# Kernel tuning notes

Hardware: AMD Instinct MI355X
Metric: run time of the kernel (lower is better)

## Reference

```python
import jax, jax.numpy as jnp
import numpy as np

N = 16384      # nodes
E = 524288     # edges (avg degree 32)
F_IN, H1, H2 = 256, 64, 32


def _spmm(edge_src, edge_dst, edge_weight, h):
    """Sparse A @ h with A given as COO edge list: out[i] = sum_{e: src==i} w_e * h[dst_e]."""
    msg = h[edge_dst] * edge_weight[:, None]          # [E, d] gather + scale
    return jax.ops.segment_sum(msg, edge_src, num_segments=N)


def setup_inputs() -> dict:
    key = jax.random.key(0)
    ks = jax.random.split(key, 9)
    x = jax.random.normal(ks[0], (N, F_IN), dtype=jnp.float32)
    edge_src = jax.random.randint(ks[1], (E,), 0, N, dtype=jnp.int32)
    edge_dst = jax.random.randint(ks[2], (E,), 0, N, dtype=jnp.int32)
    edge_weight = jax.random.uniform(ks[3], (E,), dtype=jnp.float32)
    # Xavier-uniform GCN weights
    def xavier(k, shape):
        lim = np.sqrt(6.0 / (shape[0] + shape[1])).astype(np.float32)
        return jax.random.uniform(k, shape, jnp.float32, -lim, lim)
    W1 = xavier(ks[4], (F_IN, H1))
    W2 = xavier(ks[5], (H1, H2))
    W3 = xavier(ks[6], (H1, H2))
    R = jax.random.normal(ks[7], (H2,), dtype=jnp.float32)           # DEDICOM diagonal
    M = jnp.diag(jax.random.normal(ks[8], (H2,), dtype=jnp.float32))  # initialized as diag(randn)
    return dict(x=x, edge_weight=edge_weight, W1=W1, W2=W2, W3=W3, R=R, M=M,
                edge_src=edge_src, edge_dst=edge_dst)


def reference(x, edge_weight, W1, W2, W3, R, M, edge_src, edge_dst):
    # GCN propagation A @ (X @ W); stored activations are never applied in the
    # original ConvGraph.forward, so none are applied here. Eval mode: no
    # dropout, reparameterize returns z_mean.
    h = _spmm(edge_src, edge_dst, edge_weight, x @ W1)        # [N, H1]
    z_mean = _spmm(edge_src, edge_dst, edge_weight, h @ W2)   # [N, H2]
    z_log_std = _spmm(edge_src, edge_dst, edge_weight, h @ W3)
    z = z_mean
    # DEDICOM decoder (act = identity): zt = z @ diag(R) @ M @ diag(R); out = zt @ zt.T
    zt = ((z * R[None, :]) @ M) * R[None, :]                  # diag matmuls -> elementwise scales
    adj_pred = zt @ zt.T                                      # [N, N]
    return adj_pred, z_mean, z_log_std
```

## Files before the change

kernel.cpp:

```cpp
#include <hip/hip_runtime.h>
#include <hip/hip_bf16.h>

#define NN 16384
#define NE 524288
#define FIN 256
#define HH1 64
#define HH2 32

typedef __attribute__((ext_vector_type(8))) short bf16x8;
typedef __attribute__((ext_vector_type(4))) float f32x4;

__global__ __launch_bounds__(256) void zero_ints(int* __restrict__ p, int n) {
  int i = blockIdx.x * 256 + threadIdx.x;
  if (i < n) p[i] = 0;
}

__global__ __launch_bounds__(256) void gemm_xw1(const float* __restrict__ x,
                                                const float* __restrict__ W1,
                                                float* __restrict__ H0) {
  __shared__ float xs[64][65];
  __shared__ float ws[64][65];
  const int t = threadIdx.x;
  const int row0 = blockIdx.x * 64;
  const int tr = t >> 4, tc = t & 15;
  float acc[4][4] = {};
  for (int kc = 0; kc < FIN; kc += 64) {
#pragma unroll
    for (int i = 0; i < 4; ++i) {
      int slot = t + i * 256;
      int r = slot >> 4, c4 = (slot & 15) * 4;
      float4 v = *reinterpret_cast<const float4*>(&x[(size_t)(row0 + r) * FIN + kc + c4]);
      xs[r][c4 + 0] = v.x; xs[r][c4 + 1] = v.y; xs[r][c4 + 2] = v.z; xs[r][c4 + 3] = v.w;
      float4 wv = *reinterpret_cast<const float4*>(&W1[(size_t)(kc + r) * HH1 + c4]);
      ws[r][c4 + 0] = wv.x; ws[r][c4 + 1] = wv.y; ws[r][c4 + 2] = wv.z; ws[r][c4 + 3] = wv.w;
    }
    __syncthreads();
#pragma unroll
    for (int k = 0; k < 64; ++k) {
      float a[4], b[4];
#pragma unroll
      for (int i = 0; i < 4; ++i) a[i] = xs[tr * 4 + i][k];
#pragma unroll
      for (int j = 0; j < 4; ++j) b[j] = ws[k][tc * 4 + j];
#pragma unroll
      for (int i = 0; i < 4; ++i)
#pragma unroll
        for (int j = 0; j < 4; ++j) acc[i][j] += a[i] * b[j];
    }
    __syncthreads();
  }
#pragma unroll
  for (int i = 0; i < 4; ++i) {
    float4 o; o.x = acc[i][0]; o.y = acc[i][1]; o.z = acc[i][2]; o.w = acc[i][3];
    *reinterpret_cast<float4*>(&H0[(size_t)(row0 + tr * 4 + i) * HH1 + tc * 4]) = o;
  }
}

__global__ __launch_bounds__(256) void hist_src(const int* __restrict__ src,
                                                int* __restrict__ cnt) {
  int e = blockIdx.x * 256 + threadIdx.x;
  if (e < NE) atomicAdd(&cnt[src[e]], 1);
}

__global__ __launch_bounds__(256) void scan_offsets(const int* __restrict__ cnt,
                                                    int* __restrict__ off,
                                                    int* __restrict__ cur) {
  __shared__ int wsum[4];
  __shared__ int wpre[4];
  const int t = threadIdx.x;
  const int lane = t & 63, w = t >> 6;
  int v[64];
#pragma unroll
  for (int i = 0; i < 16; ++i) {
    int4 q = reinterpret_cast<const int4*>(cnt)[t * 16 + i];
    v[i * 4 + 0] = q.x; v[i * 4 + 1] = q.y; v[i * 4 + 2] = q.z; v[i * 4 + 3] = q.w;
  }
  int s = 0;
#pragma unroll
  for (int i = 0; i < 64; ++i) s += v[i];
  int incl = s;
#pragma unroll
  for (int d = 1; d < 64; d <<= 1) {
    int n = __shfl_up(incl, d, 64);
    if (lane >= d) incl += n;
  }
  if (lane == 63) wsum[w] = incl;
  __syncthreads();
  if (t == 0) {
    int run = 0;
    for (int i = 0; i < 4; ++i) { int x = wsum[i]; wpre[i] = run; run += x; }
  }
  __syncthreads();
  int run = incl - s + wpre[w];
#pragma unroll
  for (int i = 0; i < 16; ++i) {
    int4 o;
    o.x = run; run += v[i * 4 + 0];
    o.y = run; run += v[i * 4 + 1];
    o.z = run; run += v[i * 4 + 2];
    o.w = run; run += v[i * 4 + 3];
    reinterpret_cast<int4*>(off)[t * 16 + i] = o;
    reinterpret_cast<int4*>(cur)[t * 16 + i] = o;
  }
  if (t == 255) off[NN] = run;
}

__global__ __launch_bounds__(256) void scatter_edges(const int* __restrict__ src,
                                                     const int* __restrict__ dst,
                                                     const float* __restrict__ w,
                                                     int* __restrict__ cur,
                                                     int* __restrict__ sdst,
                                                     float* __restrict__ sw) {
  int e = blockIdx.x * 256 + threadIdx.x;
  if (e < NE) {
    int s = src[e];
    int p = atomicAdd(&cur[s], 1);
    sdst[p] = dst[e];
    sw[p] = w[e];
  }
}

__global__ __launch_bounds__(256) void spmm_g(const int* __restrict__ off,
                                              const int* __restrict__ sdst,
                                              const float* __restrict__ sw,
                                              const float* __restrict__ Hin,
                                              const float* __restrict__ W2,
                                              const float* __restrict__ W3,
                                              float* __restrict__ G) {
  __shared__ float wsh[64][64];
  __shared__ float hsh[4][64];
  const int t = threadIdx.x;
  for (int i = t; i < 64 * 32; i += 256) {
    int k = i >> 5, c = i & 31;
    wsh[k][c]      = W2[i];
    wsh[k][c + 32] = W3[i];
  }
  const int node = blockIdx.x * 4 + (t >> 6);
  const int lane = t & 63;
  const int beg = off[node], end = off[node + 1];
  float acc = 0.f;
  int e = beg;
  for (; e + 4 <= end; e += 4) {
    int d0 = sdst[e], d1 = sdst[e + 1], d2 = sdst[e + 2], d3 = sdst[e + 3];
    float w0 = sw[e], w1 = sw[e + 1], w2 = sw[e + 2], w3 = sw[e + 3];
    acc += w0 * Hin[(size_t)d0 * 64 + lane];
    acc += w1 * Hin[(size_t)d1 * 64 + lane];
    acc += w2 * Hin[(size_t)d2 * 64 + lane];
    acc += w3 * Hin[(size_t)d3 * 64 + lane];
  }
  for (; e < end; ++e) acc += sw[e] * Hin[(size_t)sdst[e] * 64 + lane];
  hsh[t >> 6][lane] = acc;
  __syncthreads();
  float g = 0.f;
#pragma unroll
  for (int k = 0; k < 64; ++k) g += hsh[t >> 6][k] * wsh[k][lane];
  G[(size_t)node * 64 + lane] = g;
}

__global__ __launch_bounds__(256) void spmm_zt(const int* __restrict__ off,
                                               const int* __restrict__ sdst,
                                               const float* __restrict__ sw,
                                               const float* __restrict__ G,
                                               const float* __restrict__ R,
                                               const float* __restrict__ M,
                                               float* __restrict__ zmean,
                                               float* __restrict__ zlog,
                                               __hip_bfloat16* __restrict__ ztb) {
  __shared__ float Ms[32][33];
  __shared__ float zr[4][32];
  const int t = threadIdx.x;
  for (int i = t; i < 1024; i += 256) Ms[i >> 5][i & 31] = M[i];
  const int wv = t >> 6, lane = t & 63;
  const int node = blockIdx.x * 4 + wv;
  const int beg = off[node], end = off[node + 1];
  float acc = 0.f;
  int e = beg;
  for (; e + 4 <= end; e += 4) {
    int d0 = sdst[e], d1 = sdst[e + 1], d2 = sdst[e + 2], d3 = sdst[e + 3];
    float w0 = sw[e], w1 = sw[e + 1], w2 = sw[e + 2], w3 = sw[e + 3];
    acc += w0 * G[(size_t)d0 * 64 + lane];
    acc += w1 * G[(size_t)d1 * 64 + lane];
    acc += w2 * G[(size_t)d2 * 64 + lane];
    acc += w3 * G[(size_t)d3 * 64 + lane];
  }
  for (; e < end; ++e) acc += sw[e] * G[(size_t)sdst[e] * 64 + lane];
  if (lane < 32) {
    zmean[(size_t)node * 32 + lane] = acc;
    zr[wv][lane] = acc * R[lane];
  } else {
    zlog[(size_t)node * 32 + (lane - 32)] = acc;
  }
  __syncthreads();
  if (lane < 32) {
    float zt = 0.f;
#pragma unroll
    for (int k = 0; k < 32; ++k) zt += zr[wv][k] * Ms[k][lane];
    ztb[(size_t)node * 32 + lane] = __float2bfloat16(zt * R[lane]);
  }
}

__global__ __launch_bounds__(256) void adj_mfma(const __hip_bfloat16* __restrict__ ztb,
                                                float* __restrict__ adj) {
  __shared__ float lds[4][16][128];
  const int wave = threadIdx.x >> 6;
  const int lane = threadIdx.x & 63;
  const int l15 = lane & 15;
  const int kblk = lane >> 4;
  const int rbase = blockIdx.y * 64 + wave * 16;
  const int cbase = blockIdx.x * 128;
  const short* zs = reinterpret_cast<const short*>(ztb);

  bf16x8 b0 = *reinterpret_cast<const bf16x8*>(&zs[(size_t)(rbase + l15) * 32 + kblk * 8]);

#pragma unroll
  for (int tc = 0; tc < 8; ++tc) {
    bf16x8 a = *reinterpret_cast<const bf16x8*>(
        &zs[(size_t)(cbase + tc * 16 + l15) * 32 + kblk * 8]);
    f32x4 z4 = {0.f, 0.f, 0.f, 0.f};
    f32x4 d = __builtin_amdgcn_mfma_f32_16x16x32_bf16(a, b0, z4, 0, 0, 0);
    int unit = (tc * 4 + kblk) ^ (l15 & 7);
    *reinterpret_cast<f32x4*>(&lds[wave][l15][unit * 4]) = d;
  }

  const int j = lane & 7;
#pragma unroll
  for (int rg = 0; rg < 2; ++rg) {
    const int rl = rg * 8 + (lane >> 3);
    float* dst = &adj[(size_t)(rbase + rl) * NN + cbase];
#pragma unroll
    for (int it = 0; it < 4; ++it) {
      int unit = (it * 8 + j) ^ (rl & 7);
      f32x4 v = *reinterpret_cast<const f32x4*>(&lds[wave][rl][unit * 4]);
      *reinterpret_cast<f32x4*>(dst + it * 32 + j * 4) = v;
    }
  }
}

extern "C" void kernel_launch(void* const* d_in, const int* in_sizes, int n_in,
                              void* d_out, int out_size, void* d_ws, size_t ws_size,
                              hipStream_t stream) {
  (void)in_sizes; (void)n_in; (void)out_size; (void)ws_size;

  const float* x   = (const float*)d_in[0];
  const float* ew  = (const float*)d_in[1];
  const float* W1  = (const float*)d_in[2];
  const float* W2  = (const float*)d_in[3];
  const float* W3  = (const float*)d_in[4];
  const float* R   = (const float*)d_in[5];
  const float* M   = (const float*)d_in[6];
  const int* esrc  = (const int*)d_in[7];
  const int* edst  = (const int*)d_in[8];

  float* adj_out   = (float*)d_out;
  float* zmean_out = adj_out + (size_t)NN * NN;
  float* zlog_out  = zmean_out + (size_t)NN * HH2;

  char* p = (char*)d_ws;
  float* H0 = (float*)p;                 p += (size_t)NN * HH1 * 4;
  float* G  = (float*)p;                 p += (size_t)NN * HH1 * 4;
  __hip_bfloat16* ztb = (__hip_bfloat16*)p; p += (size_t)NN * HH2 * 2;
  int* cnt  = (int*)p;                   p += (size_t)NN * 4;
  int* off  = (int*)p;                   p += (size_t)(NN + 4) * 4;
  int* cur  = (int*)p;                   p += (size_t)NN * 4;
  int* sdst = (int*)p;                   p += (size_t)NE * 4;
  float* sw = (float*)p;                 p += (size_t)NE * 4;

  zero_ints<<<NN / 256, 256, 0, stream>>>(cnt, NN);
  gemm_xw1<<<NN / 64, 256, 0, stream>>>(x, W1, H0);
  hist_src<<<NE / 256, 256, 0, stream>>>(esrc, cnt);
  scan_offsets<<<1, 256, 0, stream>>>(cnt, off, cur);
  scatter_edges<<<NE / 256, 256, 0, stream>>>(esrc, edst, ew, cur, sdst, sw);
  spmm_g<<<NN / 4, 256, 0, stream>>>(off, sdst, sw, H0, W2, W3, G);
  spmm_zt<<<NN / 4, 256, 0, stream>>>(off, sdst, sw, G, R, M,
                                      zmean_out, zlog_out, ztb);

  dim3 g(NN / 128, NN / 64, 1);
  adj_mfma<<<g, 256, 0, stream>>>(ztb, adj_out);
}
```

Measured before the change: 324.4 us.

## Make adj kernel persistent over full row strips and fold zeroing into GEMM

The adjacency kernel now gives each block a 16-row strip across all 16384 columns, looping over 512-column chunks. Each chunk goes through a swizzled shared tile so every output row is written as long contiguous 2KB segments. The grid shrinks from 32768 small blocks to 1024, which cuts launch and tail overhead and makes the dominant store stream more sequential. The zeroing of the histogram counts is merged into the X·W1 GEMM launch as extra blocks, removing one kernel launch. The cost is two barriers per chunk and fewer blocks available to hide store latency.

Result: slower. 337.0 us (+3.9%).

```diff
diff --git a/kernel.cpp b/kernel.cpp
--- a/kernel.cpp
+++ b/kernel.cpp
@@ -10,14 +10,15 @@
 typedef __attribute__((ext_vector_type(8))) short bf16x8;
 typedef __attribute__((ext_vector_type(4))) float f32x4;
 
-__global__ __launch_bounds__(256) void zero_ints(int* __restrict__ p, int n) {
-  int i = blockIdx.x * 256 + threadIdx.x;
-  if (i < n) p[i] = 0;
-}
-
-__global__ __launch_bounds__(256) void gemm_xw1(const float* __restrict__ x,
-                                                const float* __restrict__ W1,
-                                                float* __restrict__ H0) {
+__global__ __launch_bounds__(256) void gemm_xw1_zero(const float* __restrict__ x,
+                                                     const float* __restrict__ W1,
+                                                     float* __restrict__ H0,
+                                                     int* __restrict__ cnt) {
+  if (blockIdx.x >= 256) {
+    int i = (blockIdx.x - 256) * 256 + threadIdx.x;
+    cnt[i] = 0;
+    return;
+  }
   __shared__ float xs[64][65];
   __shared__ float ws[64][65];
   const int t = threadIdx.x;
@@ -201,38 +202,41 @@
 
 __global__ __launch_bounds__(256) void adj_mfma(const __hip_bfloat16* __restrict__ ztb,
                                                 float* __restrict__ adj) {
-  __shared__ float lds[4][16][128];
-  const int wave = threadIdx.x >> 6;
-  const int lane = threadIdx.x & 63;
+  __shared__ float tile[16][512];
+  const int t = threadIdx.x;
+  const int wave = t >> 6;
+  const int lane = t & 63;
   const int l15 = lane & 15;
   const int kblk = lane >> 4;
-  const int rbase = blockIdx.y * 64 + wave * 16;
-  const int cbase = blockIdx.x * 128;
+  const int rbase = blockIdx.x * 16;
   const short* zs = reinterpret_cast<const short*>(ztb);
 
   bf16x8 b0 = *reinterpret_cast<const bf16x8*>(&zs[(size_t)(rbase + l15) * 32 + kblk * 8]);
 
-#pragma unroll
-  for (int tc = 0; tc < 8; ++tc) {
-    bf16x8 a = *reinterpret_cast<const bf16x8*>(
-        &zs[(size_t)(cbase + tc * 16 + l15) * 32 + kblk * 8]);
-    f32x4 z4 = {0.f, 0.f, 0.f, 0.f};
-    f32x4 d = __builtin_amdgcn_mfma_f32_16x16x32_bf16(a, b0, z4, 0, 0, 0);
-    int unit = (tc * 4 + kblk) ^ (l15 & 7);
-    *reinterpret_cast<f32x4*>(&lds[wave][l15][unit * 4]) = d;
-  }
-
-  const int j = lane & 7;
-#pragma unroll
-  for (int rg = 0; rg < 2; ++rg) {
-    const int rl = rg * 8 + (lane >> 3);
-    float* dst = &adj[(size_t)(rbase + rl) * NN + cbase];
-#pragma unroll
-    for (int it = 0; it < 4; ++it) {
-      int unit = (it * 8 + j) ^ (rl & 7);
-      f32x4 v = *reinterpret_cast<const f32x4*>(&lds[wave][rl][unit * 4]);
-      *reinterpret_cast<f32x4*>(dst + it * 32 + j * 4) = v;
-    }
+  const int prow = t >> 7;
+  const int pk = t & 127;
+
+  for (int cstep = 0; cstep < 32; ++cstep) {
+    const int c0 = cstep * 512;
+#pragma unroll
+    for (int tc = 0; tc < 8; ++tc) {
+      const int acol = c0 + wave * 128 + tc * 16 + l15;
+      bf16x8 a = *reinterpret_cast<const bf16x8*>(&zs[(size_t)acol * 32 + kblk * 8]);
+      f32x4 z4 = {0.f, 0.f, 0.f, 0.f};
+      f32x4 d = __builtin_amdgcn_mfma_f32_16x16x32_bf16(a, b0, z4, 0, 0, 0);
+      const int u = wave * 32 + tc * 4 + kblk;
+      const int pu = u ^ (l15 & 7);
+      *reinterpret_cast<f32x4*>(&tile[l15][pu * 4]) = d;
+    }
+    __syncthreads();
+#pragma unroll
+    for (int r = 0; r < 8; ++r) {
+      const int row = r * 2 + prow;
+      const int pu = pk ^ (row & 7);
+      f32x4 v = *reinterpret_cast<const f32x4*>(&tile[row][pu * 4]);
+      *reinterpret_cast<f32x4*>(&adj[(size_t)(rbase + row) * NN + c0 + pk * 4]) = v;
+    }
+    __syncthreads();
   }
 }
 
@@ -265,8 +269,7 @@
   int* sdst = (int*)p;                   p += (size_t)NE * 4;
   float* sw = (float*)p;                 p += (size_t)NE * 4;
 
-  zero_ints<<<NN / 256, 256, 0, stream>>>(cnt, NN);
-  gemm_xw1<<<NN / 64, 256, 0, stream>>>(x, W1, H0);
+  gemm_xw1_zero<<<320, 256, 0, stream>>>(x, W1, H0, cnt);
   hist_src<<<NE / 256, 256, 0, stream>>>(esrc, cnt);
   scan_offsets<<<1, 256, 0, stream>>>(cnt, off, cur);
   scatter_edges<<<NE / 256, 256, 0, stream>>>(esrc, edst, ew, cur, sdst, sw);
@@ -274,6 +277,5 @@
   spmm_zt<<<NN / 4, 256, 0, stream>>>(off, sdst, sw, G, R, M,
                                       zmean_out, zlog_out, ztb);
 
-  dim3 g(NN / 128, NN / 64, 1);
-  adj_mfma<<<g, 256, 0, stream>>>(ztb, adj_out);
-}
+  adj_mfma<<<NN / 16, 256, 0, stream>>>(ztb, adj_out);
+}
```
